# Optimization experiments

Measured on AMD Instinct MI355X. Metric: run time of the kernel, lower is better.

## Reference

```python
import jax, jax.numpy as jnp
import numpy as np

B, T, A, F, K, DQ, DV = 64, 1024, 128, 1024, 31, 1024, 512  # filters F == T required by source math


def setup_inputs() -> dict:
    key = jax.random.key(0)
    ks = jax.random.split(key, 8)
    s = 0.05
    return {
        "query": jax.random.normal(ks[0], (B, 1, DQ), jnp.float32),
        "value": jax.random.normal(ks[1], (B, T, DV), jnp.float32),
        "attention_weights_cat": jax.random.uniform(ks[2], (B, T, 2), jnp.float32),
        "Wq": jax.random.normal(ks[3], (DQ, A), jnp.float32) * s,
        "Wm": jax.random.normal(ks[4], (DV, A), jnp.float32) * s,
        "Wv": jax.random.normal(ks[5], (A, 1), jnp.float32) * s,
        "Wconv": jax.random.normal(ks[6], (K, 2, F), jnp.float32) * s,
        "Wloc": jax.random.normal(ks[7], (T, A), jnp.float32) * s,
    }


def reference(query, value, attention_weights_cat, Wq, Wm, Wv, Wconv, Wloc):
    # query_layer: Dense(tanh, no bias): [B,1,DQ] -> [B,1,A]
    q = jnp.tanh(jnp.einsum('bld,da->bla', query, Wq))
    # memory_layer: Dense(tanh, no bias): [B,T,DV] -> [B,T,A]
    v = jnp.tanh(jnp.einsum('btd,da->bta', value, Wm))
    # location conv (SAME, no bias): [B,T,2] -> [B,T,F]
    loc = jax.lax.conv_general_dilated(
        attention_weights_cat, Wconv, window_strides=(1,), padding='SAME',
        dimension_numbers=('NWC', 'WIO', 'NWC'))
    # source transposes [0,2,1] then Dense(T->A, tanh): [B,F,T] -> [B,F,A]
    loc = jnp.tanh(jnp.einsum('bft,ta->bfa', jnp.transpose(loc, (0, 2, 1)), Wloc))
    # additive score (F == T so broadcast add is element-aligned): [B,T,1]
    score = jnp.einsum('bta,ao->bto', jnp.tanh(q + v + loc), Wv)
    alignment = jax.nn.softmax(score, axis=1)                # softmax over time
    context = jnp.sum(alignment * v, axis=1)                  # [B,A]
    return context, jnp.transpose(alignment, (0, 2, 1))       # [B,1,T]
```

## Files before the change

### kernel.cpp

```cpp
#include <hip/hip_runtime.h>
#include <hip/hip_bf16.h>

#define BB 64
#define TT 1024
#define AA 128
#define FF 1024
#define DQ 1024
#define DV 512

typedef __bf16 bf16x8_t __attribute__((ext_vector_type(8)));
typedef __bf16 bf16x4_t __attribute__((ext_vector_type(4)));
typedef float f32x4_t __attribute__((ext_vector_type(4)));
typedef _Float16 f16x4_t __attribute__((ext_vector_type(4)));

__device__ __forceinline__ float ftanh(float x) {
    float e = __expf(2.0f * x);
    return 1.0f - 2.0f / (e + 1.0f);
}

__device__ __forceinline__ __bf16 bhi(float x) { return (__bf16)x; }
__device__ __forceinline__ __bf16 blo(float x) {
    __bf16 h = (__bf16)x;
    return (__bf16)(x - (float)h);
}

__global__ __launch_bounds__(256) void k_prep(
    const float* __restrict__ Wm, const float* __restrict__ Wconv,
    const float* __restrict__ Wloc, const float* __restrict__ query,
    const float* __restrict__ Wq,
    __bf16* __restrict__ pwmhi, __bf16* __restrict__ pwmlo,
    __bf16* __restrict__ wcthi, __bf16* __restrict__ wctlo,
    __bf16* __restrict__ pwlhi, __bf16* __restrict__ pwllo,
    float* __restrict__ q_ws) {
    __shared__ float ls[128 * 65];
    int bx = blockIdx.x, tid = threadIdx.x;
    if (bx < 16) {
        int s = bx, d0 = s * 32;
        for (int i = tid; i < 4096; i += 256) {
            int dd = i >> 7, a = i & 127;
            ls[a * 33 + dd] = Wm[(d0 + dd) * AA + a];
        }
        __syncthreads();
#pragma unroll
        for (int u = 0; u < 2; u++) {
            int pos = tid * 2 + u;
            int l15 = pos & 15, lq = (pos >> 4) & 3, g = pos >> 6;
            bf16x8_t h8, l8;
#pragma unroll
            for (int j = 0; j < 8; j++) {
                float x = ls[(g * 16 + l15) * 33 + lq * 8 + j];
                h8[j] = bhi(x);
                l8[j] = blo(x);
            }
            size_t off = (size_t)(s * 512 + pos) * 8;
            *(bf16x8_t*)(pwmhi + off) = h8;
            *(bf16x8_t*)(pwmlo + off) = l8;
        }
    } else if (bx < 24) {
        int f0 = (bx - 16) * 128;
        for (int i = tid; i < 8192; i += 256) {
            int kc = i >> 7, f = i & 127;
            ls[f * 65 + kc] = (kc < 62) ? Wconv[kc * FF + f0 + f] : 0.f;
        }
        __syncthreads();
        int f = tid >> 1, half = tid & 1;
#pragma unroll
        for (int g = 0; g < 4; g++) {
            bf16x8_t h8, l8;
#pragma unroll
            for (int j = 0; j < 8; j++) {
                float x = ls[f * 65 + half * 32 + g * 8 + j];
                h8[j] = bhi(x);
                l8[j] = blo(x);
            }
            size_t off = (size_t)(f0 + f) * 64 + half * 32 + g * 8;
            *(bf16x8_t*)(wcthi + off) = h8;
            *(bf16x8_t*)(wctlo + off) = l8;
        }
    } else if (bx < 56) {
        int s2 = bx - 24, t0 = s2 * 32;
        for (int i = tid; i < 4096; i += 256) {
            int tt = i >> 7, a = i & 127;
            ls[a * 33 + tt] = Wloc[(t0 + tt) * AA + a];
        }
        __syncthreads();
#pragma unroll
        for (int u = 0; u < 2; u++) {
            int pos = tid * 2 + u;
            int l15 = pos & 15, lq = (pos >> 4) & 3, g = pos >> 6;
            bf16x8_t h8, l8;
#pragma unroll
            for (int j = 0; j < 8; j++) {
                float x = ls[(g * 16 + l15) * 33 + lq * 8 + j];
                h8[j] = bhi(x);
                l8[j] = blo(x);
            }
            size_t off = (size_t)(s2 * 512 + pos) * 8;
            *(bf16x8_t*)(pwlhi + off) = h8;
            *(bf16x8_t*)(pwllo + off) = l8;
        }
    } else {
        int b = bx - 56;
        int a = tid & 127, half = tid >> 7;
        const float* qrow = query + b * DQ + half * 512;
        float a0 = 0.f, a1 = 0.f, a2 = 0.f, a3 = 0.f;
        for (int d = 0; d < 512; d += 4) {
            float4 qv = *(const float4*)(qrow + d);
            int dg = (half * 512 + d) * AA + a;
            a0 += qv.x * Wq[dg];
            a1 += qv.y * Wq[dg + AA];
            a2 += qv.z * Wq[dg + 2 * AA];
            a3 += qv.w * Wq[dg + 3 * AA];
        }
        ls[tid] = a0 + a1 + a2 + a3;
        __syncthreads();
        if (half == 0) q_ws[b * AA + a] = ftanh(ls[a] + ls[a + 128]);
    }
}

__global__ __launch_bounds__(256) void k_zq(
    const float* __restrict__ xcat,
    const __bf16* __restrict__ pwlhi, const __bf16* __restrict__ pwllo,
    __bf16* __restrict__ zthi, __bf16* __restrict__ ztlo) {
    int b = blockIdx.x, tid = threadIdx.x;
    __shared__ float xs0[1056], xs1[1056];
    __shared__ float zs[64 * 132];
    for (int i = tid; i < 1056; i += 256) {
        int t = i - 16;
        float2 xv = (t >= 0 && t < TT) ? *(const float2*)(xcat + (size_t)(b * TT + t) * 2)
                                       : make_float2(0.f, 0.f);
        xs0[i] = xv.x;
        xs1[i] = xv.y;
    }
    __syncthreads();
    int lane = tid & 63, wid = tid >> 6;
    int wm = wid >> 1, wn = wid & 1;
    int l15 = lane & 15, lq = lane >> 4;

    f32x4_t zacc[2][4];
#pragma unroll
    for (int mi = 0; mi < 2; mi++)
#pragma unroll
        for (int ni = 0; ni < 4; ni++) zacc[mi][ni] = (f32x4_t){0.f, 0.f, 0.f, 0.f};

    for (int s = 0; s < 32; s++) {
        int t0 = s * 32;
        bf16x8_t bh[4], bl[4];
#pragma unroll
        for (int ni = 0; ni < 4; ni++) {
            size_t poff = (size_t)((s * 8 + wn * 4 + ni) * 64 + lane) * 8;
            bh[ni] = *(const bf16x8_t*)(pwlhi + poff);
            bl[ni] = *(const bf16x8_t*)(pwllo + poff);
        }
        bf16x8_t ah[2], al[2];
#pragma unroll
        for (int mi = 0; mi < 2; mi++) {
            int kc = wm * 32 + mi * 16 + l15;
            const float* xsc = (kc & 1) ? xs1 : xs0;
            int base = t0 + lq * 8 + (kc >> 1) + 1;
#pragma unroll
            for (int j = 0; j < 8; j++) {
                float x = xsc[base + j];
                ah[mi][j] = bhi(x);
                al[mi][j] = blo(x);
            }
        }
#pragma unroll
        for (int ni = 0; ni < 4; ni++)
#pragma unroll
            for (int mi = 0; mi < 2; mi++) {
                zacc[mi][ni] = __builtin_amdgcn_mfma_f32_16x16x32_bf16(ah[mi], bh[ni], zacc[mi][ni], 0, 0, 0);
                zacc[mi][ni] = __builtin_amdgcn_mfma_f32_16x16x32_bf16(al[mi], bh[ni], zacc[mi][ni], 0, 0, 0);
                zacc[mi][ni] = __builtin_amdgcn_mfma_f32_16x16x32_bf16(ah[mi], bl[ni], zacc[mi][ni], 0, 0, 0);
            }
    }
#pragma unroll
    for (int mi = 0; mi < 2; mi++)
#pragma unroll
        for (int ni = 0; ni < 4; ni++)
#pragma unroll
            for (int r = 0; r < 4; r++)
                zs[(wm * 32 + mi * 16 + lq * 4 + r) * 132 + wn * 64 + ni * 16 + l15] = zacc[mi][ni][r];
    __syncthreads();
    int a = tid >> 1, half = tid & 1;
#pragma unroll
    for (int g = 0; g < 4; g++) {
        bf16x8_t h8, l8;
#pragma unroll
        for (int j = 0; j < 8; j++) {
            float x = zs[(half * 32 + g * 8 + j) * 132 + a];
            h8[j] = bhi(x);
            l8[j] = blo(x);
        }
        size_t off = ((size_t)b * AA + a) * 64 + half * 32 + g * 8;
        *(bf16x8_t*)(zthi + off) = h8;
        *(bf16x8_t*)(ztlo + off) = l8;
    }
}

__global__ __launch_bounds__(256, 3) void k_main(
    const float* __restrict__ value,
    const __bf16* __restrict__ pwmhi, const __bf16* __restrict__ pwmlo,
    const __bf16* __restrict__ wcthi, const __bf16* __restrict__ wctlo,
    const __bf16* __restrict__ zthi, const __bf16* __restrict__ ztlo,
    const float* __restrict__ q_ws, const float* __restrict__ Wv,
    _Float16* __restrict__ v_ws, float* __restrict__ score) {
    int b = blockIdx.x >> 4;
    int trow0 = (blockIdx.x & 15) << 6;
    int tid = threadIdx.x;
    int lane = tid & 63, wid = tid >> 6;
    int wm = wid >> 1, wn = wid & 1;
    int l15 = lane & 15, lq = lane >> 4;

    __shared__ float sc_red[128];

    f32x4_t acc[2][4];
#pragma unroll
    for (int mi = 0; mi < 2; mi++)
#pragma unroll
        for (int ni = 0; ni < 4; ni++) acc[mi][ni] = (f32x4_t){0.f, 0.f, 0.f, 0.f};

    const float* a0p = value + (size_t)(b * TT + trow0 + wm * 32 + l15) * DV + lq * 8;
    const float* a1p = a0p + (size_t)16 * DV;
    const __bf16* pbh = pwmhi + (size_t)(wn * 4 * 64 + lane) * 8;
    const __bf16* pbl = pwmlo + (size_t)(wn * 4 * 64 + lane) * 8;

    f32x4_t fa[2][2][2];
    bf16x8_t bhb[2][4], blb[2][4];

#define GL4(dst, ptr, OFF) \
    asm volatile("global_load_dwordx4 %0, %1, off offset:" OFF : "=v"(dst) : "v"(ptr))

    GL4(fa[0][0][0], a0p, "0");
    GL4(fa[0][0][1], a0p, "16");
    GL4(fa[0][1][0], a1p, "0");
    GL4(fa[0][1][1], a1p, "16");
    GL4(bhb[0][0], pbh, "0");
    GL4(bhb[0][1], pbh, "1024");
    GL4(bhb[0][2], pbh, "2048");
    GL4(bhb[0][3], pbh, "3072");
    GL4(blb[0][0], pbl, "0");
    GL4(blb[0][1], pbl, "1024");
    GL4(blb[0][2], pbl, "2048");
    GL4(blb[0][3], pbl, "3072");
    a0p += 32; a1p += 32; pbh += 4096; pbl += 4096;

#pragma unroll
    for (int it = 0; it < 16; ++it) {
        const int cur = it & 1, nxt = (it + 1) & 1;
        if (it < 15) {
            GL4(fa[nxt][0][0], a0p, "0");
            GL4(fa[nxt][0][1], a0p, "16");
            GL4(fa[nxt][1][0], a1p, "0");
            GL4(fa[nxt][1][1], a1p, "16");
            GL4(bhb[nxt][0], pbh, "0");
            GL4(bhb[nxt][1], pbh, "1024");
            GL4(bhb[nxt][2], pbh, "2048");
            GL4(bhb[nxt][3], pbh, "3072");
            GL4(blb[nxt][0], pbl, "0");
            GL4(blb[nxt][1], pbl, "1024");
            GL4(blb[nxt][2], pbl, "2048");
            GL4(blb[nxt][3], pbl, "3072");
            a0p += 32; a1p += 32; pbh += 4096; pbl += 4096;
            asm volatile("s_waitcnt vmcnt(12)");
        } else {
            asm volatile("s_waitcnt vmcnt(0)");
        }
        __builtin_amdgcn_sched_barrier(0);

        bf16x8_t ah[2], al[2];
#pragma unroll
        for (int mi = 0; mi < 2; mi++)
#pragma unroll
            for (int h = 0; h < 2; h++)
#pragma unroll
                for (int j = 0; j < 4; j++) {
                    float x = fa[cur][mi][h][j];
                    ah[mi][h * 4 + j] = bhi(x);
                    al[mi][h * 4 + j] = blo(x);
                }
#pragma unroll
        for (int mi = 0; mi < 2; mi++)
#pragma unroll
            for (int ni = 0; ni < 4; ni++) {
                acc[mi][ni] = __builtin_amdgcn_mfma_f32_16x16x32_bf16(ah[mi], bhb[cur][ni], acc[mi][ni], 0, 0, 0);
                acc[mi][ni] = __builtin_amdgcn_mfma_f32_16x16x32_bf16(al[mi], bhb[cur][ni], acc[mi][ni], 0, 0, 0);
                acc[mi][ni] = __builtin_amdgcn_mfma_f32_16x16x32_bf16(ah[mi], blb[cur][ni], acc[mi][ni], 0, 0, 0);
            }
    }
#undef GL4

    f32x4_t lacc[2][4];
#pragma unroll
    for (int mi = 0; mi < 2; mi++)
#pragma unroll
        for (int ni = 0; ni < 4; ni++) lacc[mi][ni] = (f32x4_t){0.f, 0.f, 0.f, 0.f};
#pragma unroll
    for (int kc0 = 0; kc0 < 64; kc0 += 32) {
        bf16x8_t a2h[2], a2l[2], b2h[4], b2l[4];
#pragma unroll
        for (int mi = 0; mi < 2; mi++) {
            int f = trow0 + wm * 32 + mi * 16 + l15;
            a2h[mi] = *(const bf16x8_t*)(wcthi + (size_t)f * 64 + kc0 + lq * 8);
            a2l[mi] = *(const bf16x8_t*)(wctlo + (size_t)f * 64 + kc0 + lq * 8);
        }
#pragma unroll
        for (int ni = 0; ni < 4; ni++) {
            int a = wn * 64 + ni * 16 + l15;
            size_t off = ((size_t)b * AA + a) * 64 + kc0 + lq * 8;
            b2h[ni] = *(const bf16x8_t*)(zthi + off);
            b2l[ni] = *(const bf16x8_t*)(ztlo + off);
        }
#pragma unroll
        for (int mi = 0; mi < 2; mi++)
#pragma unroll
            for (int ni = 0; ni < 4; ni++) {
                lacc[mi][ni] = __builtin_amdgcn_mfma_f32_16x16x32_bf16(a2h[mi], b2h[ni], lacc[mi][ni], 0, 0, 0);
                lacc[mi][ni] = __builtin_amdgcn_mfma_f32_16x16x32_bf16(a2l[mi], b2h[ni], lacc[mi][ni], 0, 0, 0);
                lacc[mi][ni] = __builtin_amdgcn_mfma_f32_16x16x32_bf16(a2h[mi], b2l[ni], lacc[mi][ni], 0, 0, 0);
            }
    }

    float qv[4], wv[4];
#pragma unroll
    for (int ni = 0; ni < 4; ni++) {
        int a = wn * 64 + ni * 16 + l15;
        qv[ni] = q_ws[b * AA + a];
        wv[ni] = Wv[a];
    }
#pragma unroll
    for (int mi = 0; mi < 2; mi++) {
#pragma unroll
        for (int r = 0; r < 4; r++) {
            int tl = wm * 32 + mi * 16 + lq * 4 + r;
            int t = trow0 + tl;
            float s = 0.f;
#pragma unroll
            for (int ni = 0; ni < 4; ni++) {
                float v = ftanh(acc[mi][ni][r]);
                float loc = ftanh(lacc[mi][ni][r]);
                int a = wn * 64 + ni * 16 + l15;
                v_ws[(size_t)(b * TT + t) * AA + a] = (_Float16)v;
                s += ftanh(qv[ni] + v + loc) * wv[ni];
            }
            s += __shfl_xor(s, 1, 64);
            s += __shfl_xor(s, 2, 64);
            s += __shfl_xor(s, 4, 64);
            s += __shfl_xor(s, 8, 64);
            if (l15 == 0) sc_red[wn * 64 + tl] = s;
        }
    }
    __syncthreads();
    if (tid < 64) score[b * TT + trow0 + tid] = sc_red[tid] + sc_red[64 + tid];
}

__global__ void k_softmax(const float* __restrict__ score, float* __restrict__ out_align) {
    int b = blockIdx.x, tid = threadIdx.x;
    __shared__ float red[4];
    float s[4];
#pragma unroll
    for (int i = 0; i < 4; i++) s[i] = score[b * TT + tid + i * 256];
    float m = fmaxf(fmaxf(s[0], s[1]), fmaxf(s[2], s[3]));
    for (int off = 32; off; off >>= 1) m = fmaxf(m, __shfl_xor(m, off, 64));
    int wid = tid >> 6;
    if ((tid & 63) == 0) red[wid] = m;
    __syncthreads();
    float M = fmaxf(fmaxf(red[0], red[1]), fmaxf(red[2], red[3]));
    __syncthreads();
    float e[4];
    float sum = 0.f;
#pragma unroll
    for (int i = 0; i < 4; i++) { e[i] = __expf(s[i] - M); sum += e[i]; }
    for (int off = 32; off; off >>= 1) sum += __shfl_xor(sum, off, 64);
    if ((tid & 63) == 0) red[wid] = sum;
    __syncthreads();
    float inv = 1.0f / (red[0] + red[1] + red[2] + red[3]);
#pragma unroll
    for (int i = 0; i < 4; i++) out_align[b * TT + tid + i * 256] = e[i] * inv;
}

__global__ void k_context(const float* __restrict__ align, const _Float16* __restrict__ v_ws,
                          float* __restrict__ out_ctx) {
    int b = blockIdx.y, t0 = blockIdx.x * 64, tid = threadIdx.x;
    int a0 = (tid & 31) * 4, tl = tid >> 5;
    __shared__ float sh[8 * 132];
    f32x4_t acc = (f32x4_t){0.f, 0.f, 0.f, 0.f};
    for (int tt = tl; tt < 64; tt += 8) {
        float w = align[b * TT + t0 + tt];
        f16x4_t vv = *(const f16x4_t*)(v_ws + (size_t)(b * TT + t0 + tt) * AA + a0);
        acc[0] += w * (float)vv[0];
        acc[1] += w * (float)vv[1];
        acc[2] += w * (float)vv[2];
        acc[3] += w * (float)vv[3];
    }
    *(f32x4_t*)&sh[tl * 132 + a0] = acc;
    __syncthreads();
    if (tid < 128) {
        float s = 0.f;
#pragma unroll
        for (int j = 0; j < 8; j++) s += sh[j * 132 + tid];
        atomicAdd(out_ctx + b * AA + tid, s);
    }
}

extern "C" void kernel_launch(void* const* d_in, const int* in_sizes, int n_in,
                              void* d_out, int out_size, void* d_ws, size_t ws_size,
                              hipStream_t stream) {
    const float* query = (const float*)d_in[0];
    const float* value = (const float*)d_in[1];
    const float* xcat  = (const float*)d_in[2];
    const float* Wq    = (const float*)d_in[3];
    const float* Wm    = (const float*)d_in[4];
    const float* Wv    = (const float*)d_in[5];
    const float* Wconv = (const float*)d_in[6];
    const float* Wloc  = (const float*)d_in[7];
    float* out = (float*)d_out;

    float* ws = (float*)d_ws;
    float* q_ws  = ws;
    float* sc_ws = q_ws + 8192;
    _Float16* v_ws = (_Float16*)(sc_ws + 65536);
    __bf16* pwmhi = (__bf16*)(sc_ws + 65536 + 4194304);
    __bf16* pwmlo = pwmhi + 65536;
    __bf16* wcthi = pwmlo + 65536;
    __bf16* wctlo = wcthi + 65536;
    __bf16* pwlhi = wctlo + 65536;
    __bf16* pwllo = pwlhi + 131072;
    __bf16* zthi  = pwllo + 131072;
    __bf16* ztlo  = zthi + 524288;

    (void)hipMemsetAsync(out, 0, (size_t)8192 * 4, stream);

    k_prep<<<120, 256, 0, stream>>>(Wm, Wconv, Wloc, query, Wq,
                                    pwmhi, pwmlo, wcthi, wctlo, pwlhi, pwllo, q_ws);
    k_zq<<<BB, 256, 0, stream>>>(xcat, pwlhi, pwllo, zthi, ztlo);
    k_main<<<1024, 256, 0, stream>>>(value, pwmhi, pwmlo, wcthi, wctlo, zthi, ztlo,
                                     q_ws, Wv, v_ws, sc_ws);
    k_softmax<<<BB, 256, 0, stream>>>(sc_ws, out + 8192);
    k_context<<<dim3(16, BB), 256, 0, stream>>>(out + 8192, v_ws, out);
}
```

Measured before the change: 304.7 us.

## Split k_zq across A halves and stagger K-loop start per block

k_zq now launches 128 blocks, each computing half of the A columns for one batch. This doubles parallelism on a 256-CU device that previously ran only 64 blocks. Both k_zq and k_main rotate the starting K-slice by a per-block phase, so concurrent blocks read different parts of the shared weight arrays and contend less for the same cache lines. The cost is that the x-staging in LDS is duplicated across the two halves of k_zq, and addressing in the pipelined loop becomes slightly more complex.

```diff
diff --git a/kernel.cpp b/kernel.cpp
--- a/kernel.cpp
+++ b/kernel.cpp
@@ -122,9 +122,11 @@
     const float* __restrict__ xcat,
     const __bf16* __restrict__ pwlhi, const __bf16* __restrict__ pwllo,
     __bf16* __restrict__ zthi, __bf16* __restrict__ ztlo) {
-    int b = blockIdx.x, tid = threadIdx.x;
+    int bx = blockIdx.x;
+    int b = bx & 63, ah = bx >> 6;
+    int tid = threadIdx.x;
     __shared__ float xs0[1056], xs1[1056];
-    __shared__ float zs[64 * 132];
+    __shared__ float zs[64 * 66];
     for (int i = tid; i < 1056; i += 256) {
         int t = i - 16;
         float2 xv = (t >= 0 && t < TT) ? *(const float2*)(xcat + (size_t)(b * TT + t) * 2)
@@ -137,22 +139,25 @@
     int wm = wid >> 1, wn = wid & 1;
     int l15 = lane & 15, lq = lane >> 4;
 
-    f32x4_t zacc[2][4];
+    f32x4_t zacc[2][2];
 #pragma unroll
     for (int mi = 0; mi < 2; mi++)
 #pragma unroll
-        for (int ni = 0; ni < 4; ni++) zacc[mi][ni] = (f32x4_t){0.f, 0.f, 0.f, 0.f};
-
-    for (int s = 0; s < 32; s++) {
+        for (int ni = 0; ni < 2; ni++) zacc[mi][ni] = (f32x4_t){0.f, 0.f, 0.f, 0.f};
+
+    int phase = bx & 31;
+    for (int sl = 0; sl < 32; sl++) {
+        int s = (sl + phase) & 31;
         int t0 = s * 32;
-        bf16x8_t bh[4], bl[4];
-#pragma unroll
-        for (int ni = 0; ni < 4; ni++) {
-            size_t poff = (size_t)((s * 8 + wn * 4 + ni) * 64 + lane) * 8;
+        bf16x8_t bh[2], bl[2];
+#pragma unroll
+        for (int ni = 0; ni < 2; ni++) {
+            int g = ah * 4 + wn * 2 + ni;
+            size_t poff = (size_t)((s * 8 + g) * 64 + lane) * 8;
             bh[ni] = *(const bf16x8_t*)(pwlhi + poff);
             bl[ni] = *(const bf16x8_t*)(pwllo + poff);
         }
-        bf16x8_t ah[2], al[2];
+        bf16x8_t ah_[2], al_[2];
 #pragma unroll
         for (int mi = 0; mi < 2; mi++) {
             int kc = wm * 32 + mi * 16 + l15;
@@ -161,38 +166,38 @@
 #pragma unroll
             for (int j = 0; j < 8; j++) {
                 float x = xsc[base + j];
-                ah[mi][j] = bhi(x);
-                al[mi][j] = blo(x);
-            }
-        }
-#pragma unroll
-        for (int ni = 0; ni < 4; ni++)
+                ah_[mi][j] = bhi(x);
+                al_[mi][j] = blo(x);
+            }
+        }
+#pragma unroll
+        for (int ni = 0; ni < 2; ni++)
 #pragma unroll
             for (int mi = 0; mi < 2; mi++) {
-                zacc[mi][ni] = __builtin_amdgcn_mfma_f32_16x16x32_bf16(ah[mi], bh[ni], zacc[mi][ni], 0, 0, 0);
-                zacc[mi][ni] = __builtin_amdgcn_mfma_f32_16x16x32_bf16(al[mi], bh[ni], zacc[mi][ni], 0, 0, 0);
-                zacc[mi][ni] = __builtin_amdgcn_mfma_f32_16x16x32_bf16(ah[mi], bl[ni], zacc[mi][ni], 0, 0, 0);
+                zacc[mi][ni] = __builtin_amdgcn_mfma_f32_16x16x32_bf16(ah_[mi], bh[ni], zacc[mi][ni], 0, 0, 0);
+                zacc[mi][ni] = __builtin_amdgcn_mfma_f32_16x16x32_bf16(al_[mi], bh[ni], zacc[mi][ni], 0, 0, 0);
+                zacc[mi][ni] = __builtin_amdgcn_mfma_f32_16x16x32_bf16(ah_[mi], bl[ni], zacc[mi][ni], 0, 0, 0);
             }
     }
 #pragma unroll
     for (int mi = 0; mi < 2; mi++)
 #pragma unroll
-        for (int ni = 0; ni < 4; ni++)
+        for (int ni = 0; ni < 2; ni++)
 #pragma unroll
             for (int r = 0; r < 4; r++)
-                zs[(wm * 32 + mi * 16 + lq * 4 + r) * 132 + wn * 64 + ni * 16 + l15] = zacc[mi][ni][r];
-    __syncthreads();
-    int a = tid >> 1, half = tid & 1;
-#pragma unroll
-    for (int g = 0; g < 4; g++) {
+                zs[(wm * 32 + mi * 16 + lq * 4 + r) * 66 + wn * 32 + ni * 16 + l15] = zacc[mi][ni][r];
+    __syncthreads();
+    int a_local = tid & 63, seg = tid >> 6;
+#pragma unroll
+    for (int g = 0; g < 2; g++) {
         bf16x8_t h8, l8;
 #pragma unroll
         for (int j = 0; j < 8; j++) {
-            float x = zs[(half * 32 + g * 8 + j) * 132 + a];
+            float x = zs[(seg * 16 + g * 8 + j) * 66 + a_local];
             h8[j] = bhi(x);
             l8[j] = blo(x);
         }
-        size_t off = ((size_t)b * AA + a) * 64 + half * 32 + g * 8;
+        size_t off = ((size_t)b * AA + ah * 64 + a_local) * 64 + seg * 16 + g * 8;
         *(bf16x8_t*)(zthi + off) = h8;
         *(bf16x8_t*)(ztlo + off) = l8;
     }
@@ -211,6 +216,7 @@
     int lane = tid & 63, wid = tid >> 6;
     int wm = wid >> 1, wn = wid & 1;
     int l15 = lane & 15, lq = lane >> 4;
+    int phase = (blockIdx.x + (blockIdx.x >> 4)) & 15;
 
     __shared__ float sc_red[128];
 
@@ -220,48 +226,42 @@
 #pragma unroll
         for (int ni = 0; ni < 4; ni++) acc[mi][ni] = (f32x4_t){0.f, 0.f, 0.f, 0.f};
 
-    const float* a0p = value + (size_t)(b * TT + trow0 + wm * 32 + l15) * DV + lq * 8;
-    const float* a1p = a0p + (size_t)16 * DV;
-    const __bf16* pbh = pwmhi + (size_t)(wn * 4 * 64 + lane) * 8;
-    const __bf16* pbl = pwmlo + (size_t)(wn * 4 * 64 + lane) * 8;
+    const float* a0b = value + (size_t)(b * TT + trow0 + wm * 32 + l15) * DV + lq * 8;
+    const float* a1b = a0b + (size_t)16 * DV;
+    const __bf16* pbh0 = pwmhi + (size_t)(wn * 4 * 64 + lane) * 8;
+    const __bf16* pbl0 = pwmlo + (size_t)(wn * 4 * 64 + lane) * 8;
 
     f32x4_t fa[2][2][2];
     bf16x8_t bhb[2][4], blb[2][4];
 
 #define GL4(dst, ptr, OFF) \
     asm volatile("global_load_dwordx4 %0, %1, off offset:" OFF : "=v"(dst) : "v"(ptr))
-
-    GL4(fa[0][0][0], a0p, "0");
-    GL4(fa[0][0][1], a0p, "16");
-    GL4(fa[0][1][0], a1p, "0");
-    GL4(fa[0][1][1], a1p, "16");
-    GL4(bhb[0][0], pbh, "0");
-    GL4(bhb[0][1], pbh, "1024");
-    GL4(bhb[0][2], pbh, "2048");
-    GL4(bhb[0][3], pbh, "3072");
-    GL4(blb[0][0], pbl, "0");
-    GL4(blb[0][1], pbl, "1024");
-    GL4(blb[0][2], pbl, "2048");
-    GL4(blb[0][3], pbl, "3072");
-    a0p += 32; a1p += 32; pbh += 4096; pbl += 4096;
+#define ISSUE(buf, s) { \
+    const float* _a0 = a0b + (s) * 32; \
+    const float* _a1 = a1b + (s) * 32; \
+    const __bf16* _bh = pbh0 + (size_t)(s) * 4096; \
+    const __bf16* _bl = pbl0 + (size_t)(s) * 4096; \
+    GL4(fa[buf][0][0], _a0, "0"); \
+    GL4(fa[buf][0][1], _a0, "16"); \
+    GL4(fa[buf][1][0], _a1, "0"); \
+    GL4(fa[buf][1][1], _a1, "16"); \
+    GL4(bhb[buf][0], _bh, "0"); \
+    GL4(bhb[buf][1], _bh, "1024"); \
+    GL4(bhb[buf][2], _bh, "2048"); \
+    GL4(bhb[buf][3], _bh, "3072"); \
+    GL4(blb[buf][0], _bl, "0"); \
+    GL4(blb[buf][1], _bl, "1024"); \
+    GL4(blb[buf][2], _bl, "2048"); \
+    GL4(blb[buf][3], _bl, "3072"); }
+
+    ISSUE(0, phase);
 
 #pragma unroll
     for (int it = 0; it < 16; ++it) {
         const int cur = it & 1, nxt = (it + 1) & 1;
         if (it < 15) {
-            GL4(fa[nxt][0][0], a0p, "0");
-            GL4(fa[nxt][0][1], a0p, "16");
-            GL4(fa[nxt][1][0], a1p, "0");
-            GL4(fa[nxt][1][1], a1p, "16");
-            GL4(bhb[nxt][0], pbh, "0");
-            GL4(bhb[nxt][1], pbh, "1024");
-            GL4(bhb[nxt][2], pbh, "2048");
-            GL4(bhb[nxt][3], pbh, "3072");
-            GL4(blb[nxt][0], pbl, "0");
-            GL4(blb[nxt][1], pbl, "1024");
-            GL4(blb[nxt][2], pbl, "2048");
-            GL4(blb[nxt][3], pbl, "3072");
-            a0p += 32; a1p += 32; pbh += 4096; pbl += 4096;
+            int s2 = (it + 1 + phase) & 15;
+            ISSUE(nxt, s2);
             asm volatile("s_waitcnt vmcnt(12)");
         } else {
             asm volatile("s_waitcnt vmcnt(0)");
@@ -288,6 +288,7 @@
                 acc[mi][ni] = __builtin_amdgcn_mfma_f32_16x16x32_bf16(ah[mi], blb[cur][ni], acc[mi][ni], 0, 0, 0);
             }
     }
+#undef ISSUE
 #undef GL4
 
     f32x4_t lacc[2][4];
@@ -433,7 +434,7 @@
 
     k_prep<<<120, 256, 0, stream>>>(Wm, Wconv, Wloc, query, Wq,
                                     pwmhi, pwmlo, wcthi, wctlo, pwlhi, pwllo, q_ws);
-    k_zq<<<BB, 256, 0, stream>>>(xcat, pwlhi, pwllo, zthi, ztlo);
+    k_zq<<<128, 256, 0, stream>>>(xcat, pwlhi, pwllo, zthi, ztlo);
     k_main<<<1024, 256, 0, stream>>>(value, pwmhi, pwmlo, wcthi, wctlo, zthi, ztlo,
                                      q_ws, Wv, v_ws, sc_ws);
     k_softmax<<<BB, 256, 0, stream>>>(sc_ws, out + 8192);
```

After: 286.6 us. 1.06x faster.
